# Optimization experiments

Measured on AMD Instinct MI355X. Metric: run time of the kernel, lower is better.

## Reference

```python
import jax, jax.numpy as jnp
import numpy as np

N_NODES = 10000
EPS = 1e-5


def _layernorm(x, gamma, beta):
    mu = jnp.mean(x, axis=-1, keepdims=True)
    var = jnp.mean(jnp.square(x - mu), axis=-1, keepdims=True)
    return (x - mu) * jax.lax.rsqrt(var + EPS) * gamma + beta


def _sage_pool_layer(h, src, dst, Wp, bp, Ws, Wn, b, gamma, beta):
    # DGL SAGEConv(aggregator='pool'):
    #   m_u = relu(h_u @ Wp^T + bp); h_neigh[v] = max_{u in N(v)} m_u (0 if no neighbors)
    #   rst = h @ Ws^T + h_neigh @ Wn^T + b
    m = jax.nn.relu(h @ Wp.T + bp)              # [N, d]
    msg = m[src]                                 # [E, d] gather
    agg = jax.ops.segment_max(msg, dst, num_segments=N_NODES)
    agg = jnp.where(jnp.isfinite(agg), agg, 0.0)  # isolated nodes -> 0
    rst = h @ Ws.T + agg @ Wn.T + b
    # gsage_layer: LayerNorm, then Encoder applies relu (dropout inactive in eval)
    return jax.nn.relu(_layernorm(rst, gamma, beta))


def setup_inputs() -> dict:
    key = jax.random.key(0)
    ks = jax.random.split(key, 16)
    d = 256
    E = 320000
    s = 1.0 / np.sqrt(d)
    inp = {
        "h": jax.random.normal(ks[0], (N_NODES, d), dtype=jnp.float32),
        "edge_src": jax.random.randint(ks[1], (E,), 0, N_NODES, dtype=jnp.int32),
        "edge_dst": jax.random.randint(ks[2], (E,), 0, N_NODES, dtype=jnp.int32),
    }
    for li in range(2):
        kk = jax.random.split(ks[3 + li], 3)
        inp[f"Wp{li}"] = jax.random.normal(kk[0], (d, d), dtype=jnp.float32) * s
        inp[f"bp{li}"] = jnp.zeros((d,), jnp.float32)
        inp[f"Ws{li}"] = jax.random.normal(kk[1], (d, d), dtype=jnp.float32) * s
        inp[f"Wn{li}"] = jax.random.normal(kk[2], (d, d), dtype=jnp.float32) * s
        inp[f"b{li}"] = jnp.zeros((d,), jnp.float32)
        inp[f"g{li}"] = jnp.ones((d,), jnp.float32)
        inp[f"be{li}"] = jnp.zeros((d,), jnp.float32)
    return inp


def reference(h, edge_src, edge_dst,
              Wp0, bp0, Ws0, Wn0, b0, g0, be0,
              Wp1, bp1, Ws1, Wn1, b1, g1, be1):
    h = _sage_pool_layer(h, edge_src, edge_dst, Wp0, bp0, Ws0, Wn0, b0, g0, be0)
    h = _sage_pool_layer(h, edge_src, edge_dst, Wp1, bp1, Ws1, Wn1, b1, g1, be1)
    return h
```

## Files before the change

kernel.cpp:

```cpp
#include <hip/hip_runtime.h>

#define D 256
#define CAP 128
#define ASTRIDE 280
#define LN_EPS 1e-5f

typedef short short8 __attribute__((ext_vector_type(8)));
typedef float floatx4 __attribute__((ext_vector_type(4)));

__device__ __forceinline__ unsigned short f2b(float f) {
    union { float f; unsigned int u; } x; x.f = f;
    unsigned int u = x.u + 0x7FFFu + ((x.u >> 16) & 1u);
    return (unsigned short)(u >> 16);
}

__global__ __launch_bounds__(256) void prep_kernel(
    const float* __restrict__ w0, const float* __restrict__ w1,
    const float* __restrict__ w2, const float* __restrict__ w3,
    const float* __restrict__ w4, const float* __restrict__ w5,
    unsigned short* __restrict__ wb,
    const float* __restrict__ h, unsigned short* __restrict__ hb, int nh4,
    int* __restrict__ cnt, int N)
{
    const int blk = blockIdx.x;
    const int tid = threadIdx.x;
    if (blk < 384) {
        const int wsel = blk >> 6;
        const float* src;
        switch (wsel) {
            case 0: src = w0; break; case 1: src = w1; break;
            case 2: src = w2; break; case 3: src = w3; break;
            case 4: src = w4; break; default: src = w5; break;
        }
        const int idx = (blk & 63) * 1024 + tid * 4;
        const float4 v = *(const float4*)(src + idx);
        ushort4 o;
        o.x = f2b(v.x); o.y = f2b(v.y); o.z = f2b(v.z); o.w = f2b(v.w);
        *(ushort4*)(wb + (size_t)wsel * 65536 + idx) = o;
    } else if (blk < 2884) {
        const int i = (blk - 384) * 256 + tid;
        if (i < nh4) {
            const float4 v = *(const float4*)(h + (size_t)i * 4);
            ushort4 o;
            o.x = f2b(v.x); o.y = f2b(v.y); o.z = f2b(v.z); o.w = f2b(v.w);
            *(ushort4*)(hb + (size_t)i * 4) = o;
        }
    } else {
        const int i = (blk - 2884) * 256 + tid;
        if (i < N) cnt[i] = 0;
    }
}

__global__ __launch_bounds__(256) void scatter_kernel(
    const int* __restrict__ src, const int* __restrict__ dst,
    int* __restrict__ cnt, int* __restrict__ csr, int E)
{
    int i = blockIdx.x * blockDim.x + threadIdx.x;
    const int stride = gridDim.x * blockDim.x;
    for (; i < E; i += stride) {
        const int d = dst[i];
        const int pos = atomicAdd(&cnt[d], 1);
        if (pos < CAP) csr[(size_t)d * CAP + pos] = src[i];
    }
}

__global__ __launch_bounds__(256) void gemm_relu(
    const unsigned short* __restrict__ A, const unsigned short* __restrict__ W,
    const float* __restrict__ bias, unsigned short* __restrict__ out_b, int N)
{
    const int tid = threadIdx.x;
    const int wave = tid >> 6;
    const int lane = tid & 63;
    const int quad = lane >> 4;
    const int l16 = lane & 15;
    const int row0 = blockIdx.x * 16;
    const int koff = quad * 8;

    floatx4 acc[4];
#pragma unroll
    for (int t = 0; t < 4; t++) acc[t] = (floatx4)(0.f);

    const unsigned short* aptr = A + (size_t)(row0 + l16) * D + koff;
    const unsigned short* wptr = W + (size_t)(wave * 64 + l16) * D + koff;
#pragma unroll
    for (int k0 = 0; k0 < D; k0 += 32) {
        const short8 av = *(const short8*)(aptr + k0);
        const short8 b0 = *(const short8*)(wptr + k0);
        const short8 b1 = *(const short8*)(wptr + 16 * D + k0);
        const short8 b2 = *(const short8*)(wptr + 32 * D + k0);
        const short8 b3 = *(const short8*)(wptr + 48 * D + k0);
        acc[0] = __builtin_amdgcn_mfma_f32_16x16x32_bf16(av, b0, acc[0], 0, 0, 0);
        acc[1] = __builtin_amdgcn_mfma_f32_16x16x32_bf16(av, b1, acc[1], 0, 0, 0);
        acc[2] = __builtin_amdgcn_mfma_f32_16x16x32_bf16(av, b2, acc[2], 0, 0, 0);
        acc[3] = __builtin_amdgcn_mfma_f32_16x16x32_bf16(av, b3, acc[3], 0, 0, 0);
    }

#pragma unroll
    for (int t = 0; t < 4; t++) {
        const float bcol = bias[wave * 64 + t * 16 + l16];
#pragma unroll
        for (int r = 0; r < 4; r++) {
            const int rg = row0 + quad * 4 + r;
            const int col = wave * 64 + t * 16 + l16;
            out_b[(size_t)rg * D + col] = f2b(fmaxf(acc[t][r] + bcol, 0.f));
        }
    }
}

__global__ __launch_bounds__(256) void gemm_ln_pool(
    const unsigned short* __restrict__ A, const unsigned short* __restrict__ Wself,
    const unsigned short* __restrict__ Wneigh,
    const unsigned short* __restrict__ mpool,
    const int* __restrict__ cnt, const int* __restrict__ csr,
    const float* __restrict__ bias,
    const float* __restrict__ gamma, const float* __restrict__ beta,
    unsigned short* __restrict__ out_b, float* __restrict__ out_f, int N)
{
    __shared__ unsigned short aggS[16 * ASTRIDE];
    __shared__ float redS[4][16], redS2[4][16], muA[16], rsA[16];

    const int tid = threadIdx.x;
    const int wave = tid >> 6;
    const int lane = tid & 63;
    const int quad = lane >> 4;
    const int l16 = lane & 15;
    const int row0 = blockIdx.x * 16;
    const int koff = quad * 8;

    floatx4 acc[4];
#pragma unroll
    for (int t = 0; t < 4; t++) acc[t] = (floatx4)(0.f);

    {
        const unsigned short* aptr = A + (size_t)(row0 + l16) * D + koff;
        const unsigned short* wptr = Wself + (size_t)(wave * 64 + l16) * D + koff;
#pragma unroll
        for (int k0 = 0; k0 < D; k0 += 32) {
            const short8 av = *(const short8*)(aptr + k0);
            const short8 b0 = *(const short8*)(wptr + k0);
            const short8 b1 = *(const short8*)(wptr + 16 * D + k0);
            const short8 b2 = *(const short8*)(wptr + 32 * D + k0);
            const short8 b3 = *(const short8*)(wptr + 48 * D + k0);
            acc[0] = __builtin_amdgcn_mfma_f32_16x16x32_bf16(av, b0, acc[0], 0, 0, 0);
            acc[1] = __builtin_amdgcn_mfma_f32_16x16x32_bf16(av, b1, acc[1], 0, 0, 0);
            acc[2] = __builtin_amdgcn_mfma_f32_16x16x32_bf16(av, b2, acc[2], 0, 0, 0);
            acc[3] = __builtin_amdgcn_mfma_f32_16x16x32_bf16(av, b3, acc[3], 0, 0, 0);
        }
    }

#pragma unroll
    for (int rr = 0; rr < 4; rr++) {
        const int rl = wave * 4 + rr;
        const int rg = row0 + rl;
        const int deg = min(cnt[rg], CAP);
        const int* bk = csr + (size_t)rg * CAP;
        ushort4 mx; mx.x = 0; mx.y = 0; mx.z = 0; mx.w = 0;
        int i = 0;
        for (; i + 4 <= deg; i += 4) {
            const int s0 = bk[i], s1 = bk[i + 1], s2 = bk[i + 2], s3 = bk[i + 3];
            const ushort4 a0 = *(const ushort4*)(mpool + (size_t)s0 * D + lane * 4);
            const ushort4 a1 = *(const ushort4*)(mpool + (size_t)s1 * D + lane * 4);
            const ushort4 a2 = *(const ushort4*)(mpool + (size_t)s2 * D + lane * 4);
            const ushort4 a3 = *(const ushort4*)(mpool + (size_t)s3 * D + lane * 4);
            mx.x = max(max((int)mx.x, (int)a0.x), max(max((int)a1.x, (int)a2.x), (int)a3.x));
            mx.y = max(max((int)mx.y, (int)a0.y), max(max((int)a1.y, (int)a2.y), (int)a3.y));
            mx.z = max(max((int)mx.z, (int)a0.z), max(max((int)a1.z, (int)a2.z), (int)a3.z));
            mx.w = max(max((int)mx.w, (int)a0.w), max(max((int)a1.w, (int)a2.w), (int)a3.w));
        }
        for (; i < deg; i++) {
            const ushort4 a = *(const ushort4*)(mpool + (size_t)bk[i] * D + lane * 4);
            mx.x = max((int)mx.x, (int)a.x);
            mx.y = max((int)mx.y, (int)a.y);
            mx.z = max((int)mx.z, (int)a.z);
            mx.w = max((int)mx.w, (int)a.w);
        }
        *(ushort4*)&aggS[rl * ASTRIDE + lane * 4] = mx;
    }
    __syncthreads();

    {
        const unsigned short* wptr = Wneigh + (size_t)(wave * 64 + l16) * D + koff;
#pragma unroll
        for (int k0 = 0; k0 < D; k0 += 32) {
            const short8 av = *(const short8*)&aggS[l16 * ASTRIDE + koff + k0];
            const short8 b0 = *(const short8*)(wptr + k0);
            const short8 b1 = *(const short8*)(wptr + 16 * D + k0);
            const short8 b2 = *(const short8*)(wptr + 32 * D + k0);
            const short8 b3 = *(const short8*)(wptr + 48 * D + k0);
            acc[0] = __builtin_amdgcn_mfma_f32_16x16x32_bf16(av, b0, acc[0], 0, 0, 0);
            acc[1] = __builtin_amdgcn_mfma_f32_16x16x32_bf16(av, b1, acc[1], 0, 0, 0);
            acc[2] = __builtin_amdgcn_mfma_f32_16x16x32_bf16(av, b2, acc[2], 0, 0, 0);
            acc[3] = __builtin_amdgcn_mfma_f32_16x16x32_bf16(av, b3, acc[3], 0, 0, 0);
        }
    }

    float bcol[4];
#pragma unroll
    for (int t = 0; t < 4; t++) bcol[t] = bias[wave * 64 + t * 16 + l16];
#pragma unroll
    for (int t = 0; t < 4; t++)
#pragma unroll
        for (int r = 0; r < 4; r++) acc[t][r] += bcol[t];

#pragma unroll
    for (int r = 0; r < 4; r++) {
        float s = 0.f, s2 = 0.f;
#pragma unroll
        for (int t = 0; t < 4; t++) {
            const float v = acc[t][r];
            s += v; s2 += v * v;
        }
        s += __shfl_xor(s, 1);  s2 += __shfl_xor(s2, 1);
        s += __shfl_xor(s, 2);  s2 += __shfl_xor(s2, 2);
        s += __shfl_xor(s, 4);  s2 += __shfl_xor(s2, 4);
        s += __shfl_xor(s, 8);  s2 += __shfl_xor(s2, 8);
        if (l16 == 0) {
            redS[wave][quad * 4 + r] = s;
            redS2[wave][quad * 4 + r] = s2;
        }
    }
    __syncthreads();
    if (tid < 16) {
        const float S  = redS[0][tid] + redS[1][tid] + redS[2][tid] + redS[3][tid];
        const float S2 = redS2[0][tid] + redS2[1][tid] + redS2[2][tid] + redS2[3][tid];
        const float mu = S * (1.f / D);
        float var = S2 * (1.f / D) - mu * mu;
        var = fmaxf(var, 0.f);
        muA[tid] = mu;
        rsA[tid] = rsqrtf(var + LN_EPS);
    }
    __syncthreads();

    float gcol[4], becol[4];
#pragma unroll
    for (int t = 0; t < 4; t++) {
        gcol[t] = gamma[wave * 64 + t * 16 + l16];
        becol[t] = beta[wave * 64 + t * 16 + l16];
    }
#pragma unroll
    for (int r = 0; r < 4; r++) {
        const int rl = quad * 4 + r;
        const int rg = row0 + rl;
        const float mu = muA[rl];
        const float rs = rsA[rl];
#pragma unroll
        for (int t = 0; t < 4; t++) {
            const int col = wave * 64 + t * 16 + l16;
            float o = (acc[t][r] - mu) * rs * gcol[t] + becol[t];
            o = fmaxf(o, 0.f);
            if (out_f) out_f[(size_t)rg * D + col] = o;
            else       out_b[(size_t)rg * D + col] = f2b(o);
        }
    }
}

extern "C" void kernel_launch(void* const* d_in, const int* in_sizes, int n_in,
                              void* d_out, int out_size, void* d_ws, size_t ws_size,
                              hipStream_t stream) {
    const float* h    = (const float*)d_in[0];
    const int*   esrc = (const int*)d_in[1];
    const int*   edst = (const int*)d_in[2];
    const float* Wp0  = (const float*)d_in[3];
    const float* bp0  = (const float*)d_in[4];
    const float* Ws0  = (const float*)d_in[5];
    const float* Wn0  = (const float*)d_in[6];
    const float* b0   = (const float*)d_in[7];
    const float* g0   = (const float*)d_in[8];
    const float* be0  = (const float*)d_in[9];
    const float* Wp1  = (const float*)d_in[10];
    const float* bp1  = (const float*)d_in[11];
    const float* Ws1  = (const float*)d_in[12];
    const float* Wn1  = (const float*)d_in[13];
    const float* b1   = (const float*)d_in[14];
    const float* g1   = (const float*)d_in[15];
    const float* be1  = (const float*)d_in[16];

    const int N = in_sizes[0] / D;
    const int E = in_sizes[1];
    const size_t ND = (size_t)N * D;

    unsigned short* hb  = (unsigned short*)d_ws;
    unsigned short* mb  = hb + ND;
    unsigned short* h1b = mb + ND;
    unsigned short* wb  = h1b + ND;
    int* cnt = (int*)(wb + 6 * 65536);
    int* csr = cnt + N;

    unsigned short* wpb0 = wb + 0 * 65536;
    unsigned short* wsb0 = wb + 1 * 65536;
    unsigned short* wnb0 = wb + 2 * 65536;
    unsigned short* wpb1 = wb + 3 * 65536;
    unsigned short* wsb1 = wb + 4 * 65536;
    unsigned short* wnb1 = wb + 5 * 65536;

    const int gblocks = N / 16;
    const int zblocks = (N + 255) / 256;
    const int pgrid = 384 + 2500 + zblocks;

    prep_kernel<<<pgrid, 256, 0, stream>>>(Wp0, Ws0, Wn0, Wp1, Ws1, Wn1, wb,
                                           h, hb, (int)(ND / 4), cnt, N);
    scatter_kernel<<<256, 256, 0, stream>>>(esrc, edst, cnt, csr, E);

    gemm_relu<<<gblocks, 256, 0, stream>>>(hb, wpb0, bp0, mb, N);
    gemm_ln_pool<<<gblocks, 256, 0, stream>>>(hb, wsb0, wnb0, mb, cnt, csr,
                                              b0, g0, be0, h1b, nullptr, N);

    gemm_relu<<<gblocks, 256, 0, stream>>>(h1b, wpb1, bp1, mb, N);
    gemm_ln_pool<<<gblocks, 256, 0, stream>>>(h1b, wsb1, wnb1, mb, cnt, csr,
                                              b1, g1, be1, nullptr, (float*)d_out, N);
}
```

Baseline: 244.1 us.

## Fuse edge scatter into first pool GEMM and batch neighbor gathers across rows

The edge-to-CSR scatter now runs in extra blocks appended to the first gemm_relu launch, so it overlaps with the projection GEMM and one launch goes away. The prep kernel uses a grid-stride loop for the bf16 conversion of h and zeroes a sentinel row appended to the pooled-message buffer. The pool kernel stages each row's neighbor indices in shared memory, padded with the zero sentinel row, and gathers four rows times four neighbors per iteration to raise memory-level parallelism. It also adds an occupancy hint of three blocks per SM. The cost is wasted gathers on padding when degrees within a wave differ, plus extra shared memory.

```diff
diff --git a/kernel.cpp b/kernel.cpp
--- a/kernel.cpp
+++ b/kernel.cpp
@@ -20,7 +20,7 @@
     const float* __restrict__ w4, const float* __restrict__ w5,
     unsigned short* __restrict__ wb,
     const float* __restrict__ h, unsigned short* __restrict__ hb, int nh4,
-    int* __restrict__ cnt, int N)
+    int* __restrict__ cnt, unsigned short* __restrict__ mb, int N)
 {
     const int blk = blockIdx.x;
     const int tid = threadIdx.x;
@@ -37,37 +37,41 @@
         ushort4 o;
         o.x = f2b(v.x); o.y = f2b(v.y); o.z = f2b(v.z); o.w = f2b(v.w);
         *(ushort4*)(wb + (size_t)wsel * 65536 + idx) = o;
-    } else if (blk < 2884) {
-        const int i = (blk - 384) * 256 + tid;
-        if (i < nh4) {
+    } else if (blk < 1024) {
+        int i = (blk - 384) * 256 + tid;
+        const int stride = 640 * 256;
+        for (; i < nh4; i += stride) {
             const float4 v = *(const float4*)(h + (size_t)i * 4);
             ushort4 o;
             o.x = f2b(v.x); o.y = f2b(v.y); o.z = f2b(v.z); o.w = f2b(v.w);
             *(ushort4*)(hb + (size_t)i * 4) = o;
         }
+    } else if (blk < 1064) {
+        const int i = (blk - 1024) * 256 + tid;
+        if (i < N) cnt[i] = 0;
     } else {
-        const int i = (blk - 2884) * 256 + tid;
-        if (i < N) cnt[i] = 0;
-    }
-}
-
-__global__ __launch_bounds__(256) void scatter_kernel(
-    const int* __restrict__ src, const int* __restrict__ dst,
-    int* __restrict__ cnt, int* __restrict__ csr, int E)
-{
-    int i = blockIdx.x * blockDim.x + threadIdx.x;
-    const int stride = gridDim.x * blockDim.x;
-    for (; i < E; i += stride) {
-        const int d = dst[i];
-        const int pos = atomicAdd(&cnt[d], 1);
-        if (pos < CAP) csr[(size_t)d * CAP + pos] = src[i];
+        mb[(size_t)N * D + tid] = 0;
     }
 }
 
 __global__ __launch_bounds__(256) void gemm_relu(
     const unsigned short* __restrict__ A, const unsigned short* __restrict__ W,
-    const float* __restrict__ bias, unsigned short* __restrict__ out_b, int N)
+    const float* __restrict__ bias, unsigned short* __restrict__ out_b, int N,
+    const int* __restrict__ esrc, const int* __restrict__ edst,
+    int* __restrict__ cnt, int* __restrict__ csr, int E, int ngemm)
 {
+    if ((int)blockIdx.x >= ngemm) {
+        const int nsb = gridDim.x - ngemm;
+        int i = ((int)blockIdx.x - ngemm) * 256 + threadIdx.x;
+        const int stride = nsb * 256;
+        for (; i < E; i += stride) {
+            const int d = edst[i];
+            const int pos = atomicAdd(&cnt[d], 1);
+            if (pos < CAP) csr[(size_t)d * CAP + pos] = esrc[i];
+        }
+        return;
+    }
+
     const int tid = threadIdx.x;
     const int wave = tid >> 6;
     const int lane = tid & 63;
@@ -107,7 +111,7 @@
     }
 }
 
-__global__ __launch_bounds__(256) void gemm_ln_pool(
+__global__ __launch_bounds__(256, 3) void gemm_ln_pool(
     const unsigned short* __restrict__ A, const unsigned short* __restrict__ Wself,
     const unsigned short* __restrict__ Wneigh,
     const unsigned short* __restrict__ mpool,
@@ -116,6 +120,7 @@
     const float* __restrict__ gamma, const float* __restrict__ beta,
     unsigned short* __restrict__ out_b, float* __restrict__ out_f, int N)
 {
+    __shared__ int idxS[16][CAP];
     __shared__ unsigned short aggS[16 * ASTRIDE];
     __shared__ float redS[4][16], redS2[4][16], muA[16], rsA[16];
 
@@ -126,6 +131,19 @@
     const int l16 = lane & 15;
     const int row0 = blockIdx.x * 16;
     const int koff = quad * 8;
+    const int rbase = wave * 4;
+
+    int degs[4];
+#pragma unroll
+    for (int rr = 0; rr < 4; rr++) degs[rr] = min(cnt[row0 + rbase + rr], CAP);
+    int P = max(max(degs[0], degs[1]), max(degs[2], degs[3]));
+    P = (P + 3) & ~3;
+#pragma unroll
+    for (int rr = 0; rr < 4; rr++) {
+        const int rg = row0 + rbase + rr;
+        for (int i = lane; i < P; i += 64)
+            idxS[rbase + rr][i] = (i < degs[rr]) ? csr[(size_t)rg * CAP + i] : N;
+    }
 
     floatx4 acc[4];
 #pragma unroll
@@ -148,33 +166,34 @@
         }
     }
 
-#pragma unroll
-    for (int rr = 0; rr < 4; rr++) {
-        const int rl = wave * 4 + rr;
-        const int rg = row0 + rl;
-        const int deg = min(cnt[rg], CAP);
-        const int* bk = csr + (size_t)rg * CAP;
-        ushort4 mx; mx.x = 0; mx.y = 0; mx.z = 0; mx.w = 0;
-        int i = 0;
-        for (; i + 4 <= deg; i += 4) {
-            const int s0 = bk[i], s1 = bk[i + 1], s2 = bk[i + 2], s3 = bk[i + 3];
-            const ushort4 a0 = *(const ushort4*)(mpool + (size_t)s0 * D + lane * 4);
-            const ushort4 a1 = *(const ushort4*)(mpool + (size_t)s1 * D + lane * 4);
-            const ushort4 a2 = *(const ushort4*)(mpool + (size_t)s2 * D + lane * 4);
-            const ushort4 a3 = *(const ushort4*)(mpool + (size_t)s3 * D + lane * 4);
-            mx.x = max(max((int)mx.x, (int)a0.x), max(max((int)a1.x, (int)a2.x), (int)a3.x));
-            mx.y = max(max((int)mx.y, (int)a0.y), max(max((int)a1.y, (int)a2.y), (int)a3.y));
-            mx.z = max(max((int)mx.z, (int)a0.z), max(max((int)a1.z, (int)a2.z), (int)a3.z));
-            mx.w = max(max((int)mx.w, (int)a0.w), max(max((int)a1.w, (int)a2.w), (int)a3.w));
-        }
-        for (; i < deg; i++) {
-            const ushort4 a = *(const ushort4*)(mpool + (size_t)bk[i] * D + lane * 4);
-            mx.x = max((int)mx.x, (int)a.x);
-            mx.y = max((int)mx.y, (int)a.y);
-            mx.z = max((int)mx.z, (int)a.z);
-            mx.w = max((int)mx.w, (int)a.w);
-        }
-        *(ushort4*)&aggS[rl * ASTRIDE + lane * 4] = mx;
+    {
+        ushort4 mx[4];
+#pragma unroll
+        for (int rr = 0; rr < 4; rr++) { mx[rr].x = 0; mx[rr].y = 0; mx[rr].z = 0; mx[rr].w = 0; }
+        for (int i = 0; i < P; i += 4) {
+            ushort4 av[4][4];
+#pragma unroll
+            for (int rr = 0; rr < 4; rr++) {
+#pragma unroll
+                for (int u = 0; u < 4; u++) {
+                    const int j = idxS[rbase + rr][i + u];
+                    av[rr][u] = *(const ushort4*)(mpool + (size_t)j * D + lane * 4);
+                }
+            }
+#pragma unroll
+            for (int rr = 0; rr < 4; rr++) {
+#pragma unroll
+                for (int u = 0; u < 4; u++) {
+                    mx[rr].x = (unsigned short)max((int)mx[rr].x, (int)av[rr][u].x);
+                    mx[rr].y = (unsigned short)max((int)mx[rr].y, (int)av[rr][u].y);
+                    mx[rr].z = (unsigned short)max((int)mx[rr].z, (int)av[rr][u].z);
+                    mx[rr].w = (unsigned short)max((int)mx[rr].w, (int)av[rr][u].w);
+                }
+            }
+        }
+#pragma unroll
+        for (int rr = 0; rr < 4; rr++)
+            *(ushort4*)&aggS[(rbase + rr) * ASTRIDE + lane * 4] = mx[rr];
     }
     __syncthreads();
 
@@ -281,7 +300,7 @@
 
     unsigned short* hb  = (unsigned short*)d_ws;
     unsigned short* mb  = hb + ND;
-    unsigned short* h1b = mb + ND;
+    unsigned short* h1b = mb + ND + D;
     unsigned short* wb  = h1b + ND;
     int* cnt = (int*)(wb + 6 * 65536);
     int* csr = cnt + N;
@@ -294,18 +313,18 @@
     unsigned short* wnb1 = wb + 5 * 65536;
 
     const int gblocks = N / 16;
-    const int zblocks = (N + 255) / 256;
-    const int pgrid = 384 + 2500 + zblocks;
-
-    prep_kernel<<<pgrid, 256, 0, stream>>>(Wp0, Ws0, Wn0, Wp1, Ws1, Wn1, wb,
-                                           h, hb, (int)(ND / 4), cnt, N);
-    scatter_kernel<<<256, 256, 0, stream>>>(esrc, edst, cnt, csr, E);
-
-    gemm_relu<<<gblocks, 256, 0, stream>>>(hb, wpb0, bp0, mb, N);
+    const int sblocks = 128;
+
+    prep_kernel<<<1065, 256, 0, stream>>>(Wp0, Ws0, Wn0, Wp1, Ws1, Wn1, wb,
+                                          h, hb, (int)(ND / 4), cnt, mb, N);
+
+    gemm_relu<<<gblocks + sblocks, 256, 0, stream>>>(hb, wpb0, bp0, mb, N,
+                                                     esrc, edst, cnt, csr, E, gblocks);
     gemm_ln_pool<<<gblocks, 256, 0, stream>>>(hb, wsb0, wnb0, mb, cnt, csr,
                                               b0, g0, be0, h1b, nullptr, N);
 
-    gemm_relu<<<gblocks, 256, 0, stream>>>(h1b, wpb1, bp1, mb, N);
+    gemm_relu<<<gblocks, 256, 0, stream>>>(h1b, wpb1, bp1, mb, N,
+                                           esrc, edst, cnt, csr, 0, gblocks);
     gemm_ln_pool<<<gblocks, 256, 0, stream>>>(h1b, wsb1, wnb1, mb, cnt, csr,
                                               b1, g1, be1, nullptr, (float*)d_out, N);
 }
```

Result: faster. 234.9 us (-3.8%).
